# Kernel optimization log

Hardware: AMD Instinct MI355X
Metric: run time of the kernel (lower is better)

The kernel has to match this reference:

```python
import jax, jax.numpy as jnp
import numpy as np

B, TA, TV, D, H = 4, 1024, 1024, 512, 8
HD = D // H
SCALE = HD ** -0.5
LN_EPS = 1e-5


def setup_inputs() -> dict:
    key = jax.random.key(0)
    ks = jax.random.split(key, 16)
    init = lambda k, shape, s: (jax.random.normal(k, shape, jnp.float32) * s)
    inp = {
        'q': jax.random.normal(ks[0], (B, TA, D), jnp.float32),
        'k': jax.random.normal(ks[1], (B, TV, D), jnp.float32),
        'v': jax.random.normal(ks[2], (B, TV, D), jnp.float32),
        'guide_map': jax.random.uniform(ks[3], (B, TA, TV), jnp.float32),
        'Wq': init(ks[4], (D, D), D ** -0.5), 'bq': jnp.zeros((D,), jnp.float32),
        'Wk': init(ks[5], (D, D), D ** -0.5), 'bk': jnp.zeros((D,), jnp.float32),
        'Wv': init(ks[6], (D, D), D ** -0.5), 'bv': jnp.zeros((D,), jnp.float32),
        'Wo': init(ks[7], (D, D), D ** -0.5), 'bo': jnp.zeros((D,), jnp.float32),
        'ln_gamma': jnp.ones((D,), jnp.float32),
        'ln_beta': jnp.zeros((D,), jnp.float32),
        'gate': jnp.zeros((1,), jnp.float32),
        'bias_scale': jnp.array(10.0, jnp.float32),
    }
    return inp


def layer_norm(x, gamma, beta):
    mu = jnp.mean(x, axis=-1, keepdims=True)
    var = jnp.mean(jnp.square(x - mu), axis=-1, keepdims=True)
    return (x - mu) * jax.lax.rsqrt(var + LN_EPS) * gamma + beta


def reference(q, k, v, guide_map, Wq, bq, Wk, bk, Wv, bv, Wo, bo, ln_gamma, ln_beta, gate, bias_scale):
    # project and split heads: [B, H, T, hd]
    Q = (q @ Wq.T + bq).reshape(B, TA, H, HD).transpose(0, 2, 1, 3)
    K = (k @ Wk.T + bk).reshape(B, TV, H, HD).transpose(0, 2, 1, 3)
    V = (v @ Wv.T + bv).reshape(B, TV, H, HD).transpose(0, 2, 1, 3)
    scores = jnp.einsum('bhqd,bhkd->bhqk', Q, K) * SCALE
    # transport bias, broadcast over heads (guide_map is [B,Ta,Tv])
    transport_bias = jnp.log(guide_map + 1e-8) * jax.nn.softplus(bias_scale)
    scores = scores + transport_bias[:, None, :, :]
    attn = jax.nn.softmax(scores, axis=-1)  # dropout is identity in eval
    context = jnp.einsum('bhqk,bhkd->bhqd', attn, V)
    context = context.transpose(0, 2, 1, 3).reshape(B, TA, D)
    out = context @ Wo.T + bo
    return layer_norm(q + jax.nn.sigmoid(gate) * out, ln_gamma, ln_beta)
```

## Files before the change

kernel.cpp:

```cpp
#include <hip/hip_runtime.h>
#include <hip/hip_bf16.h>
#include <math.h>

typedef __bf16 bf16_t;
typedef _Float16 hf16_t;
typedef bf16_t bf16x8 __attribute__((ext_vector_type(8)));
typedef hf16_t hf16x8 __attribute__((ext_vector_type(8)));
typedef float f32x4 __attribute__((ext_vector_type(4)));

#define B_  4
#define TA_ 1024
#define TV_ 1024
#define D_  512
#define H_  8
#define HD_ 64
#define SCALE_ 0.125f

__device__ inline void g2l16(const void* g, void* l) {
    __builtin_amdgcn_global_load_lds(
        (const __attribute__((address_space(1))) void*)g,
        (__attribute__((address_space(3))) void*)l, 16, 0, 0);
}

template <int CTRL>
__device__ inline float dppmov(float x) {
    int xi = __float_as_int(x);
    return __int_as_float(__builtin_amdgcn_update_dpp(xi, xi, CTRL, 0xF, 0xF, false));
}
__device__ inline float row16_max(float x) {
    x = fmaxf(x, dppmov<0xB1>(x));
    x = fmaxf(x, dppmov<0x4E>(x));
    x = fmaxf(x, dppmov<0x141>(x));
    x = fmaxf(x, dppmov<0x140>(x));
    return x;
}
__device__ inline float row16_sum(float x) {
    x += dppmov<0xB1>(x);
    x += dppmov<0x4E>(x);
    x += dppmov<0x141>(x);
    x += dppmov<0x140>(x);
    return x;
}

__global__ __launch_bounds__(256) void prep_all(
    const float* __restrict__ G, hf16_t* __restrict__ bias_t,
    const float* __restrict__ q, const float* __restrict__ k, const float* __restrict__ v,
    const float* __restrict__ Wq, const float* __restrict__ Wk,
    const float* __restrict__ Wv, const float* __restrict__ Wo,
    bf16_t* __restrict__ qb, bf16_t* __restrict__ kb, bf16_t* __restrict__ vb,
    bf16_t* __restrict__ Wb)
{
    const int tid = threadIdx.x;
    if (blockIdx.x < 1024) {
        __shared__ float Gt[64][68];
        const int kt = blockIdx.x & 15, q64 = (blockIdx.x >> 4) & 15, b = blockIdx.x >> 8;
        const int row = tid >> 4, col4 = (tid & 15) * 4;
        #pragma unroll
        for (int it = 0; it < 4; ++it) {
            int r = it * 16 + row;
            f32x4 g = *(const f32x4*)(G + ((size_t)(b * TA_ + q64 * 64 + r)) * TV_ + kt * 64 + col4);
            *(f32x4*)&Gt[r][col4] = g;
        }
        __syncthreads();
        const int lane = tid & 63, wave = tid >> 6, quad = lane >> 4, l16 = lane & 15;
        hf16x8 lo, hi;
        #pragma unroll
        for (int ct = 0; ct < 4; ++ct) {
            #pragma unroll
            for (int r = 0; r < 4; ++r) {
                float gv = Gt[wave * 16 + quad * 4 + r][ct * 16 + l16];
                float lb = __logf(gv + 1e-8f);
                int idx = ct * 4 + r;
                if (idx < 8) lo[idx] = (hf16_t)lb; else hi[idx - 8] = (hf16_t)lb;
            }
        }
        size_t doff = ((((size_t)b * 16 + kt) * 16 + q64) * 256 + tid) * 16;
        *(hf16x8*)(bias_t + doff) = lo;
        *(hf16x8*)(bias_t + doff + 8) = hi;
    } else {
        const size_t i = ((size_t)(blockIdx.x - 1024) * 256 + tid) * 8;
        const float* src; bf16_t* dst; size_t off;
        const size_t M2 = (size_t)1 << 21;
        if (i < M2)          { src = q; dst = qb; off = i; }
        else if (i < 2 * M2) { src = k; dst = kb; off = i - M2; }
        else if (i < 3 * M2) { src = v; dst = vb; off = i - 2 * M2; }
        else {
            size_t j = i - 3 * M2;
            int wsel = (int)(j >> 18); off = j & 262143;
            src = (wsel == 0) ? Wq : (wsel == 1) ? Wk : (wsel == 2) ? Wv : Wo;
            dst = Wb + ((size_t)wsel << 18);
        }
        f32x4 a = *(const f32x4*)(src + off), c = *(const f32x4*)(src + off + 4);
        bf16x8 r;
        #pragma unroll
        for (int t = 0; t < 4; ++t) { r[t] = (bf16_t)a[t]; r[t + 4] = (bf16_t)c[t]; }
        *(bf16x8*)(dst + off) = r;
    }
}

__device__ inline void gemm128_core(
    const bf16_t* __restrict__ X, const bf16_t* __restrict__ W,
    int mbase, int nbase, bf16_t (*__restrict__ Asm)[128 * 32],
    bf16_t (*__restrict__ Bsm)[128 * 32], f32x4 acc[4][4])
{
    const int tid  = threadIdx.x;
    const int wave = tid >> 6, lane = tid & 63;
    const int quad = lane >> 4, l16 = lane & 15;
    const int wm = wave & 1, wn = wave >> 1;
    const int srow = lane >> 2;
    const int scol = (lane & 3) * 8;

    auto stage = [&](int kt, int buf) {
        const int k0 = kt * 32;
        #pragma unroll
        for (int i = 0; i < 2; ++i) {
            const int row = wave * 32 + i * 16;
            g2l16(X + (size_t)(mbase + row + srow) * D_ + k0 + scol,
                  &Asm[buf][row * 32] + (size_t)lane * 8);
            g2l16(W + (size_t)(nbase + row + srow) * D_ + k0 + scol,
                  &Bsm[buf][row * 32] + (size_t)lane * 8);
        }
    };

    stage(0, 0);
    __syncthreads();
    for (int kt = 0; kt < 16; ++kt) {
        const int buf = kt & 1;
        if (kt < 15) stage(kt + 1, buf ^ 1);
        bf16x8 af[4], bf_[4];
        #pragma unroll
        for (int t = 0; t < 4; ++t) {
            af[t]  = *(const bf16x8*)&Asm[buf][(wm * 64 + t * 16 + l16) * 32 + quad * 8];
            bf_[t] = *(const bf16x8*)&Bsm[buf][(wn * 64 + t * 16 + l16) * 32 + quad * 8];
        }
        #pragma unroll
        for (int mt = 0; mt < 4; ++mt) {
            #pragma unroll
            for (int nt = 0; nt < 4; ++nt)
                acc[mt][nt] = __builtin_amdgcn_mfma_f32_16x16x32_bf16(af[mt], bf_[nt], acc[mt][nt], 0, 0, 0);
        }
        __syncthreads();
    }
}

__global__ __launch_bounds__(256) void gemm_qkv(
    const bf16_t* __restrict__ qb, const bf16_t* __restrict__ kb, const bf16_t* __restrict__ vb,
    const bf16_t* __restrict__ Wb,
    const float* __restrict__ bq, const float* __restrict__ bk, const float* __restrict__ bv,
    bf16_t* __restrict__ Qp, bf16_t* __restrict__ Kp, bf16_t* __restrict__ Vt)
{
    __shared__ bf16_t Asm[2][128 * 32];
    __shared__ bf16_t Bsm[2][128 * 32];

    const int tid  = threadIdx.x;
    const int wave = tid >> 6, lane = tid & 63;
    const int quad = lane >> 4, l16 = lane & 15;
    const int wm = wave & 1, wn = wave >> 1;
    const int mbase = blockIdx.x * 128, nbase = blockIdx.y * 128;
    const int z = blockIdx.z;

    const bf16_t* X   = (z == 0) ? qb : (z == 1) ? kb : vb;
    const float* bias = (z == 0) ? bq : (z == 1) ? bk : bv;
    const bf16_t* W   = Wb + ((size_t)z << 18);

    f32x4 acc[4][4] = {};
    gemm128_core(X, W, mbase, nbase, Asm, Bsm, acc);

    bf16_t* out = (z == 0) ? Qp : (z == 1) ? Kp : Vt;
    #pragma unroll
    for (int mt = 0; mt < 4; ++mt) {
        #pragma unroll
        for (int nt = 0; nt < 4; ++nt) {
            #pragma unroll
            for (int r = 0; r < 4; ++r) {
                int m = mbase + wm * 64 + mt * 16 + quad * 4 + r;
                int n = nbase + wn * 64 + nt * 16 + l16;
                float val = acc[mt][nt][r] + bias[n];
                int b = m >> 10, t = m & 1023, h = n >> 6, hd = n & 63;
                if (z != 2)
                    out[(((size_t)(b * H_ + h) * TA_) + t) * HD_ + hd] = (bf16_t)val;
                else
                    out[((size_t)(b * H_ + h) * HD_ + hd) * TV_ + t] = (bf16_t)val;
            }
        }
    }
}

__global__ __launch_bounds__(256) void gemm_out(
    const bf16_t* __restrict__ ctx, const bf16_t* __restrict__ Wob,
    const float* __restrict__ bo, float* __restrict__ op)
{
    __shared__ bf16_t Asm[2][128 * 32];
    __shared__ bf16_t Bsm[2][128 * 32];

    const int tid  = threadIdx.x;
    const int wave = tid >> 6, lane = tid & 63;
    const int quad = lane >> 4, l16 = lane & 15;
    const int wm = wave & 1, wn = wave >> 1;
    const int mbase = blockIdx.x * 128, nbase = blockIdx.y * 128;

    f32x4 acc[4][4] = {};
    gemm128_core(ctx, Wob, mbase, nbase, Asm, Bsm, acc);

    #pragma unroll
    for (int mt = 0; mt < 4; ++mt) {
        #pragma unroll
        for (int nt = 0; nt < 4; ++nt) {
            #pragma unroll
            for (int r = 0; r < 4; ++r) {
                int m = mbase + wm * 64 + mt * 16 + quad * 4 + r;
                int n = nbase + wn * 64 + nt * 16 + l16;
                op[(size_t)m * D_ + n] = acc[mt][nt][r] + bo[n];
            }
        }
    }
}

__global__ __launch_bounds__(256) void attn_kernel(
    const bf16_t* __restrict__ Qp, const bf16_t* __restrict__ Kp,
    const bf16_t* __restrict__ Vt, const hf16_t* __restrict__ bias_t,
    const float* __restrict__ bias_scale, bf16_t* __restrict__ ctx)
{
    __shared__ bf16_t Ksm[2][64][72];
    __shared__ bf16_t Vsm[2][64][72];
    __shared__ bf16_t Plds[4][16][72];

    const int tid  = threadIdx.x;
    const int wave = tid >> 6, lane = tid & 63;
    const int quad = lane >> 4, l16 = lane & 15;
    const int bh = blockIdx.x, b = bh >> 3;
    const int q64 = blockIdx.y;
    const int qbase = q64 * 64 + wave * 16;
    const int rsub = lane >> 3, csub = lane & 7;

    const float sp = log1pf(__expf(bias_scale[0]));

    bf16x8 aq[2];
    #pragma unroll
    for (int s = 0; s < 2; ++s)
        aq[s] = *(const bf16x8*)(Qp + ((size_t)bh * TA_ + qbase + l16) * HD_ + s * 32 + quad * 8);

    f32x4 o[4] = {};
    float m_[4], l_[4];
    #pragma unroll
    for (int i = 0; i < 4; ++i) { m_[i] = -1e30f; l_[i] = 0.f; }

    auto issue_kv = [&](int kt, bf16x8 kr[2], bf16x8 vr[2]) {
        const int kbase = kt * 64;
        #pragma unroll
        for (int i = 0; i < 2; ++i) {
            int row = wave * 16 + i * 8 + rsub;
            kr[i] = *(const bf16x8*)(Kp + ((size_t)bh * TV_ + kbase + row) * HD_ + csub * 8);
            vr[i] = *(const bf16x8*)(Vt + ((size_t)bh * HD_ + row) * TV_ + kbase + csub * 8);
        }
    };
    auto write_kv = [&](int buf, bf16x8 kr[2], bf16x8 vr[2]) {
        #pragma unroll
        for (int i = 0; i < 2; ++i) {
            int row = wave * 16 + i * 8 + rsub;
            *(bf16x8*)&Ksm[buf][row][csub * 8] = kr[i];
            *(bf16x8*)&Vsm[buf][row][csub * 8] = vr[i];
        }
    };

    const hf16_t* bias_base = bias_t + (((size_t)b * 16 * 16 + q64) * 256 + tid) * 16;
    auto bias_ld = [&](int kt, hf16x8& lo, hf16x8& hi) {
        const hf16_t* bp = bias_base + (size_t)kt * 65536;
        lo = *(const hf16x8*)bp;
        hi = *(const hf16x8*)(bp + 8);
    };
    hf16x8 b0lo, b0hi, b1lo, b1hi;
    bias_ld(0, b0lo, b0hi);
    bias_ld(1, b1lo, b1hi);

    {
        bf16x8 kr[2], vr[2];
        issue_kv(0, kr, vr);
        write_kv(0, kr, vr);
    }
    __syncthreads();

    auto tile_body = [&](int kt, int buf, hf16x8& slo, hf16x8& shi) {
        bf16x8 krn[2], vrn[2];
        if (kt < 15) issue_kv(kt + 1, krn, vrn);
        hf16x8 clo = slo, chi = shi;
        if (kt < 14) bias_ld(kt + 2, slo, shi);

        f32x4 st[4];
        #pragma unroll
        for (int ct = 0; ct < 4; ++ct) {
            f32x4 acc = {};
            #pragma unroll
            for (int s = 0; s < 2; ++s) {
                bf16x8 bk = *(const bf16x8*)&Ksm[buf][ct * 16 + l16][s * 32 + quad * 8];
                acc = __builtin_amdgcn_mfma_f32_16x16x32_bf16(aq[s], bk, acc, 0, 0, 0);
            }
            st[ct] = acc;
        }
        float sv[4][4], mx[4];
        #pragma unroll
        for (int r = 0; r < 4; ++r) mx[r] = -1e30f;
        #pragma unroll
        for (int ct = 0; ct < 4; ++ct) {
            #pragma unroll
            for (int r = 0; r < 4; ++r) {
                int idx = ct * 4 + r;
                float lb = (idx < 8) ? (float)clo[idx] : (float)chi[idx - 8];
                float val = fmaf(lb, sp, st[ct][r] * SCALE_);
                sv[ct][r] = val;
                mx[r] = fmaxf(mx[r], val);
            }
        }
        float alpha[4];
        #pragma unroll
        for (int r = 0; r < 4; ++r) {
            mx[r] = row16_max(mx[r]);
            float mn = fmaxf(m_[r], mx[r]);
            alpha[r] = __expf(m_[r] - mn);
            m_[r] = mn;
        }
        #pragma unroll
        for (int ct = 0; ct < 4; ++ct) {
            #pragma unroll
            for (int r = 0; r < 4; ++r)
                sv[ct][r] = __expf(sv[ct][r] - m_[r]);
        }
        #pragma unroll
        for (int r = 0; r < 4; ++r) {
            float lsum = row16_sum(sv[0][r] + sv[1][r] + sv[2][r] + sv[3][r]);
            l_[r] = l_[r] * alpha[r] + lsum;
        }
        #pragma unroll
        for (int ct = 0; ct < 4; ++ct) {
            #pragma unroll
            for (int r = 0; r < 4; ++r)
                Plds[wave][quad * 4 + r][ct * 16 + l16] = (bf16_t)sv[ct][r];
        }
        #pragma unroll
        for (int dt = 0; dt < 4; ++dt) {
            #pragma unroll
            for (int r = 0; r < 4; ++r) o[dt][r] *= alpha[r];
        }
        #pragma unroll
        for (int s = 0; s < 2; ++s) {
            bf16x8 ap = *(const bf16x8*)&Plds[wave][l16][s * 32 + quad * 8];
            #pragma unroll
            for (int dt = 0; dt < 4; ++dt) {
                bf16x8 bv = *(const bf16x8*)&Vsm[buf][dt * 16 + l16][s * 32 + quad * 8];
                o[dt] = __builtin_amdgcn_mfma_f32_16x16x32_bf16(ap, bv, o[dt], 0, 0, 0);
            }
        }
        if (kt < 15) write_kv(buf ^ 1, krn, vrn);
        __syncthreads();
    };

    #pragma unroll 1
    for (int kt2 = 0; kt2 < 16; kt2 += 2) {
        tile_body(kt2,     0, b0lo, b0hi);
        tile_body(kt2 + 1, 1, b1lo, b1hi);
    }

    const int h = bh & 7;
    #pragma unroll
    for (int dt = 0; dt < 4; ++dt) {
        #pragma unroll
        for (int r = 0; r < 4; ++r) {
            int qrow = q64 * 64 + wave * 16 + quad * 4 + r;
            float v = o[dt][r] / l_[r];
            ctx[((size_t)b * TA_ + qrow) * D_ + h * HD_ + dt * 16 + l16] = (bf16_t)v;
        }
    }
}

__global__ __launch_bounds__(256) void ln_kernel(
    const float* __restrict__ q, const float* __restrict__ outp,
    const float* __restrict__ gamma, const float* __restrict__ beta,
    const float* __restrict__ gate, float* __restrict__ y)
{
    const int row = blockIdx.x, tid = threadIdx.x;
    const float sg = 1.f / (1.f + __expf(-gate[0]));
    const size_t base = (size_t)row * D_;
    float x0 = q[base + tid]       + sg * outp[base + tid];
    float x1 = q[base + tid + 256] + sg * outp[base + tid + 256];
    float s = x0 + x1, sq = x0 * x0 + x1 * x1;
    #pragma unroll
    for (int off = 1; off < 64; off <<= 1) {
        s  += __shfl_xor(s,  off, 64);
        sq += __shfl_xor(sq, off, 64);
    }
    __shared__ float ss[4], sqq[4];
    if ((tid & 63) == 0) { ss[tid >> 6] = s; sqq[tid >> 6] = sq; }
    __syncthreads();
    s  = ss[0] + ss[1] + ss[2] + ss[3];
    sq = sqq[0] + sqq[1] + sqq[2] + sqq[3];
    const float mu = s * (1.f / D_);
    const float var = sq * (1.f / D_) - mu * mu;
    const float rstd = rsqrtf(var + 1e-5f);
    y[base + tid]       = (x0 - mu) * rstd * gamma[tid] + beta[tid];
    y[base + tid + 256] = (x1 - mu) * rstd * gamma[tid + 256] + beta[tid + 256];
}

extern "C" void kernel_launch(void* const* d_in, const int* in_sizes, int n_in,
                              void* d_out, int out_size, void* d_ws, size_t ws_size,
                              hipStream_t stream) {
    const float* q       = (const float*)d_in[0];
    const float* k       = (const float*)d_in[1];
    const float* v       = (const float*)d_in[2];
    const float* guide   = (const float*)d_in[3];
    const float* Wq      = (const float*)d_in[4];
    const float* bq      = (const float*)d_in[5];
    const float* Wk      = (const float*)d_in[6];
    const float* bk      = (const float*)d_in[7];
    const float* Wv      = (const float*)d_in[8];
    const float* bv      = (const float*)d_in[9];
    const float* Wo      = (const float*)d_in[10];
    const float* bo      = (const float*)d_in[11];
    const float* gamma   = (const float*)d_in[12];
    const float* beta    = (const float*)d_in[13];
    const float* gate    = (const float*)d_in[14];
    const float* bscale  = (const float*)d_in[15];

    char* w = (char*)d_ws;
    bf16_t* qb     = (bf16_t*)(w);
    bf16_t* kb     = (bf16_t*)(w + (4u  << 20));
    bf16_t* vb     = (bf16_t*)(w + (8u  << 20));
    bf16_t* Wb     = (bf16_t*)(w + (12u << 20));
    bf16_t* Qp     = (bf16_t*)(w + (14u << 20));
    bf16_t* Kp     = (bf16_t*)(w + (18u << 20));
    bf16_t* Vt     = (bf16_t*)(w + (22u << 20));
    bf16_t* ctx    = (bf16_t*)(w + (26u << 20));
    hf16_t* bias_t = (hf16_t*)(w + (30u << 20));
    float*  op     = (float*) (w);

    prep_all<<<4608, 256, 0, stream>>>(guide, bias_t, q, k, v, Wq, Wk, Wv, Wo, qb, kb, vb, Wb);
    gemm_qkv<<<dim3(32, 4, 3), 256, 0, stream>>>(qb, kb, vb, Wb, bq, bk, bv, Qp, Kp, Vt);
    attn_kernel<<<dim3(32, 16), 256, 0, stream>>>(Qp, Kp, Vt, bias_t, bscale, ctx);
    gemm_out<<<dim3(32, 4), 256, 0, stream>>>(ctx, Wb + ((size_t)3 << 18), bo, op);
    ln_kernel<<<4096, 256, 0, stream>>>(q, op, gamma, beta, gate, (float*)d_out);
}
```

Measured before the change: 182.3 us.

## Split attention KV range across two blocks and merge with combine kernel

The attention kernel now splits the 16 key tiles into two halves via a third grid dimension. This doubles the block count from 512 to 1024 and gives more waves to fill the CUs. Each half writes unnormalized bf16 partial outputs plus per-row max and sum, and a new combine kernel merges them with log-sum-exp rescaling. The out-projection also now stores bf16 instead of fp32 to cut traffic into the layernorm. Costs: an extra launch, partial-buffer traffic, and precision loss from the bf16 partials and bf16 projection output.

After: 182.7 us. Within noise of the previous version (+0.2%).

```diff
diff --git a/kernel.cpp b/kernel.cpp
--- a/kernel.cpp
+++ b/kernel.cpp
@@ -188,7 +188,7 @@
 
 __global__ __launch_bounds__(256) void gemm_out(
     const bf16_t* __restrict__ ctx, const bf16_t* __restrict__ Wob,
-    const float* __restrict__ bo, float* __restrict__ op)
+    const float* __restrict__ bo, bf16_t* __restrict__ op)
 {
     __shared__ bf16_t Asm[2][128 * 32];
     __shared__ bf16_t Bsm[2][128 * 32];
@@ -210,7 +210,7 @@
             for (int r = 0; r < 4; ++r) {
                 int m = mbase + wm * 64 + mt * 16 + quad * 4 + r;
                 int n = nbase + wn * 64 + nt * 16 + l16;
-                op[(size_t)m * D_ + n] = acc[mt][nt][r] + bo[n];
+                op[(size_t)m * D_ + n] = (bf16_t)(acc[mt][nt][r] + bo[n]);
             }
         }
     }
@@ -219,7 +219,8 @@
 __global__ __launch_bounds__(256) void attn_kernel(
     const bf16_t* __restrict__ Qp, const bf16_t* __restrict__ Kp,
     const bf16_t* __restrict__ Vt, const hf16_t* __restrict__ bias_t,
-    const float* __restrict__ bias_scale, bf16_t* __restrict__ ctx)
+    const float* __restrict__ bias_scale,
+    bf16_t* __restrict__ Opart, float* __restrict__ mpart, float* __restrict__ lpart)
 {
     __shared__ bf16_t Ksm[2][64][72];
     __shared__ bf16_t Vsm[2][64][72];
@@ -230,6 +231,8 @@
     const int quad = lane >> 4, l16 = lane & 15;
     const int bh = blockIdx.x, b = bh >> 3;
     const int q64 = blockIdx.y;
+    const int z = blockIdx.z;
+    const int t0 = z * 8;
     const int qbase = q64 * 64 + wave * 16;
     const int rsub = lane >> 3, csub = lane & 7;
 
@@ -270,21 +273,22 @@
         hi = *(const hf16x8*)(bp + 8);
     };
     hf16x8 b0lo, b0hi, b1lo, b1hi;
-    bias_ld(0, b0lo, b0hi);
-    bias_ld(1, b1lo, b1hi);
+    bias_ld(t0, b0lo, b0hi);
+    bias_ld(t0 + 1, b1lo, b1hi);
 
     {
         bf16x8 kr[2], vr[2];
-        issue_kv(0, kr, vr);
+        issue_kv(t0, kr, vr);
         write_kv(0, kr, vr);
     }
     __syncthreads();
 
-    auto tile_body = [&](int kt, int buf, hf16x8& slo, hf16x8& shi) {
+    auto tile_body = [&](int lk, int buf, hf16x8& slo, hf16x8& shi) {
+        const int kt = t0 + lk;
         bf16x8 krn[2], vrn[2];
-        if (kt < 15) issue_kv(kt + 1, krn, vrn);
+        if (lk < 7) issue_kv(kt + 1, krn, vrn);
         hf16x8 clo = slo, chi = shi;
-        if (kt < 14) bias_ld(kt + 2, slo, shi);
+        if (lk < 6) bias_ld(kt + 2, slo, shi);
 
         f32x4 st[4];
         #pragma unroll
@@ -350,38 +354,90 @@
                 o[dt] = __builtin_amdgcn_mfma_f32_16x16x32_bf16(ap, bv, o[dt], 0, 0, 0);
             }
         }
-        if (kt < 15) write_kv(buf ^ 1, krn, vrn);
+        if (lk < 7) write_kv(buf ^ 1, krn, vrn);
         __syncthreads();
     };
 
     #pragma unroll 1
-    for (int kt2 = 0; kt2 < 16; kt2 += 2) {
-        tile_body(kt2,     0, b0lo, b0hi);
-        tile_body(kt2 + 1, 1, b1lo, b1hi);
-    }
-
-    const int h = bh & 7;
+    for (int kk = 0; kk < 8; kk += 2) {
+        tile_body(kk,     0, b0lo, b0hi);
+        tile_body(kk + 1, 1, b1lo, b1hi);
+    }
+
+    const size_t blk = (size_t)bh * 16 + q64;
+    bf16x8 plo, phi;
     #pragma unroll
     for (int dt = 0; dt < 4; ++dt) {
         #pragma unroll
         for (int r = 0; r < 4; ++r) {
+            int idx = dt * 4 + r;
+            if (idx < 8) plo[idx] = (bf16_t)o[dt][r]; else phi[idx - 8] = (bf16_t)o[dt][r];
+        }
+    }
+    size_t poff = (((size_t)z * 512 + blk) * 256 + tid) * 16;
+    *(bf16x8*)(Opart + poff) = plo;
+    *(bf16x8*)(Opart + poff + 8) = phi;
+    if (l16 == 0) {
+        #pragma unroll
+        for (int r = 0; r < 4; ++r) {
+            int row = wave * 16 + quad * 4 + r;
+            mpart[((size_t)z * 512 + blk) * 64 + row] = m_[r];
+            lpart[((size_t)z * 512 + blk) * 64 + row] = l_[r];
+        }
+    }
+}
+
+__global__ __launch_bounds__(256) void attn_combine(
+    const bf16_t* __restrict__ Opart, const float* __restrict__ mpart,
+    const float* __restrict__ lpart, bf16_t* __restrict__ ctx)
+{
+    const int tid  = threadIdx.x;
+    const int wave = tid >> 6, lane = tid & 63;
+    const int quad = lane >> 4, l16 = lane & 15;
+    const int bh = blockIdx.x, b = bh >> 3, h = bh & 7;
+    const int q64 = blockIdx.y;
+    const size_t blk = (size_t)bh * 16 + q64;
+
+    size_t p0 = (blk * 256 + tid) * 16;
+    size_t p1 = (((size_t)512 + blk) * 256 + tid) * 16;
+    bf16x8 a0 = *(const bf16x8*)(Opart + p0), a1 = *(const bf16x8*)(Opart + p0 + 8);
+    bf16x8 c0 = *(const bf16x8*)(Opart + p1), c1 = *(const bf16x8*)(Opart + p1 + 8);
+
+    float s0[4], s1[4];
+    #pragma unroll
+    for (int r = 0; r < 4; ++r) {
+        int row = wave * 16 + quad * 4 + r;
+        float m0 = mpart[blk * 64 + row], m1 = mpart[(512 + blk) * 64 + row];
+        float l0 = lpart[blk * 64 + row], l1 = lpart[(512 + blk) * 64 + row];
+        float mm = fmaxf(m0, m1);
+        float e0 = __expf(m0 - mm), e1 = __expf(m1 - mm);
+        float L = l0 * e0 + l1 * e1;
+        s0[r] = e0 / L; s1[r] = e1 / L;
+    }
+    #pragma unroll
+    for (int dt = 0; dt < 4; ++dt) {
+        #pragma unroll
+        for (int r = 0; r < 4; ++r) {
+            int idx = dt * 4 + r;
+            float v0 = (idx < 8) ? (float)a0[idx] : (float)a1[idx - 8];
+            float v1 = (idx < 8) ? (float)c0[idx] : (float)c1[idx - 8];
+            float v = v0 * s0[r] + v1 * s1[r];
             int qrow = q64 * 64 + wave * 16 + quad * 4 + r;
-            float v = o[dt][r] / l_[r];
             ctx[((size_t)b * TA_ + qrow) * D_ + h * HD_ + dt * 16 + l16] = (bf16_t)v;
         }
     }
 }
 
 __global__ __launch_bounds__(256) void ln_kernel(
-    const float* __restrict__ q, const float* __restrict__ outp,
+    const float* __restrict__ q, const bf16_t* __restrict__ outp,
     const float* __restrict__ gamma, const float* __restrict__ beta,
     const float* __restrict__ gate, float* __restrict__ y)
 {
     const int row = blockIdx.x, tid = threadIdx.x;
     const float sg = 1.f / (1.f + __expf(-gate[0]));
     const size_t base = (size_t)row * D_;
-    float x0 = q[base + tid]       + sg * outp[base + tid];
-    float x1 = q[base + tid + 256] + sg * outp[base + tid + 256];
+    float x0 = q[base + tid]       + sg * (float)outp[base + tid];
+    float x1 = q[base + tid + 256] + sg * (float)outp[base + tid + 256];
     float s = x0 + x1, sq = x0 * x0 + x1 * x1;
     #pragma unroll
     for (int off = 1; off < 64; off <<= 1) {
@@ -430,11 +486,15 @@
     bf16_t* Vt     = (bf16_t*)(w + (22u << 20));
     bf16_t* ctx    = (bf16_t*)(w + (26u << 20));
     hf16_t* bias_t = (hf16_t*)(w + (30u << 20));
-    float*  op     = (float*) (w);
+    bf16_t* Opart  = (bf16_t*)(w + (38u << 20));
+    float*  mpart  = (float*) (w + (46u << 20));
+    float*  lpart  = (float*) (w + (47u << 20));
+    bf16_t* op     = (bf16_t*)(w);
 
     prep_all<<<4608, 256, 0, stream>>>(guide, bias_t, q, k, v, Wq, Wk, Wv, Wo, qb, kb, vb, Wb);
     gemm_qkv<<<dim3(32, 4, 3), 256, 0, stream>>>(qb, kb, vb, Wb, bq, bk, bv, Qp, Kp, Vt);
-    attn_kernel<<<dim3(32, 16), 256, 0, stream>>>(Qp, Kp, Vt, bias_t, bscale, ctx);
+    attn_kernel<<<dim3(32, 16, 2), 256, 0, stream>>>(Qp, Kp, Vt, bias_t, bscale, Opart, mpart, lpart);
+    attn_combine<<<dim3(32, 16), 256, 0, stream>>>(Opart, mpart, lpart, ctx);
     gemm_out<<<dim3(32, 4), 256, 0, stream>>>(ctx, Wb + ((size_t)3 << 18), bo, op);
     ln_kernel<<<4096, 256, 0, stream>>>(q, op, gamma, beta, gate, (float*)d_out);
 }
```
